# Kernel tuning notes

Measured on AMD Instinct MI355X. Metric: run time of the kernel, lower is better.

## Reference

```python
import jax, jax.numpy as jnp
import numpy as np

T, B, I, H = 512, 64, 1024, 1024


def setup_inputs() -> dict:
    key = jax.random.key(0)
    ks = jax.random.split(key, 9)
    u = lambda k, shape: jax.random.uniform(k, shape, jnp.float32, -0.05, 0.05)
    return {
        "x": jax.random.normal(ks[0], (T, B, I), jnp.float32),
        "h0": jnp.zeros((B, H), jnp.float32),
        "c0": jnp.zeros((B, H), jnp.float32),
        "W_f": u(ks[1], (I + H, H)), "b_f": u(ks[2], (H,)),
        "W_i": u(ks[3], (I + H, H)), "b_i": u(ks[4], (H,)),
        "W_C": u(ks[5], (I + H, H)), "b_C": u(ks[6], (H,)),
        "W_o": u(ks[7], (I + H, H)), "b_o": u(ks[8], (H,)),
    }


def reference(x, h0, c0, W_f, b_f, W_i, b_i, W_C, b_C, W_o, b_o):
    # Fuse the 4 gate projections into one GEMM: W is [(H_prev + I), 4H]
    W = jnp.concatenate([W_f, W_i, W_C, W_o], axis=1)  # [I+H, 4H]
    b = jnp.concatenate([b_f, b_i, b_C, b_o], axis=0)  # [4H]
    Hn = h0.shape[1]

    def step(carry, x_t):
        h_t1, c_t1 = carry
        xh = jnp.concatenate([h_t1, x_t], axis=1)  # [B, H+I]
        gates = xh @ W + b                          # [B, 4H]
        f_t = jax.nn.sigmoid(gates[:, 0 * Hn:1 * Hn])
        i_t = jax.nn.sigmoid(gates[:, 1 * Hn:2 * Hn])
        g_t = jnp.tanh(gates[:, 2 * Hn:3 * Hn])
        o_t = jax.nn.sigmoid(gates[:, 3 * Hn:4 * Hn])
        c_t = f_t * c_t1 + i_t * g_t
        h_t = o_t * jnp.tanh(c_t)
        return (h_t, c_t), h_t

    (h_last, c_last), h_seq = jax.lax.scan(step, (h0, c0), x)
    return h_seq, h_last, c_last
```

## Files before the change

kernel.cpp:

```cpp
#include <hip/hip_runtime.h>

typedef unsigned short u16;
typedef unsigned int   u32;
typedef unsigned long long u64;
typedef __attribute__((ext_vector_type(8))) __bf16 bf16x8;
typedef __attribute__((ext_vector_type(4))) float  f32x4;

#define NWG    128
#define TSTEPS 512

__device__ __forceinline__ u16 f2bf(float f) {
  union { float f; u32 u; } v; v.f = f;
  return (u16)((v.u + 0x7FFFu + ((v.u >> 16) & 1u)) >> 16);
}
__device__ __forceinline__ float sigf(float x)     { return 1.f / (1.f + __expf(-x)); }
__device__ __forceinline__ float tanhfast(float x) { return 2.f / (1.f + __expf(-2.f * x)) - 1.f; }

__global__ void convert_x_kernel(const float* __restrict__ x, u16* __restrict__ xb, long n) {
  long i = (long)(blockIdx.x * blockDim.x + threadIdx.x) * 4;
  long stride = (long)gridDim.x * blockDim.x * 4;
  for (; i < n; i += stride) {
    float4 v = *reinterpret_cast<const float4*>(x + i);
    ushort4 o; o.x = f2bf(v.x); o.y = f2bf(v.y); o.z = f2bf(v.z); o.w = f2bf(v.w);
    *reinterpret_cast<ushort4*>(xb + i) = o;
  }
}

__global__ void convert_h0_tiled(const float* __restrict__ h0, u16* __restrict__ hb) {
  int gid = blockIdx.x * blockDim.x + threadIdx.x;
  int row = gid >> 9;
  int k0  = (gid & 511) << 1;
  float a = h0[row * 1024 + k0];
  float b = h0[row * 1024 + k0 + 1];
  int off = ((row >> 4) * 32 + (k0 >> 5)) * 512 + (row & 15) * 32 + ((k0 >> 3) & 3) * 8 + (k0 & 7);
  u32 hv = (u32)f2bf(a) | ((u32)f2bf(b) << 16);
  *((u32*)hb + (off >> 1)) = hv;
}

__global__ void arrange_w_kernel(const float* __restrict__ Wf, const float* __restrict__ Wi,
                                 const float* __restrict__ Wc, const float* __restrict__ Wo,
                                 u16* __restrict__ wfrag) {
  __shared__ float lds[4][512][8];
  const int n = blockIdx.x >> 2;
  const int w = blockIdx.x & 3;
  const int tid = threadIdx.x;
  #pragma unroll
  for (int g = 0; g < 4; ++g) {
    const float* W = (g == 0) ? Wf : (g == 1) ? Wi : (g == 2) ? Wc : Wo;
    for (int it = 0; it < 16; ++it) {
      int e = it * 256 + tid;
      int kk = e >> 3, jj = e & 7;
      lds[g][kk][jj] = W[(size_t)(w * 512 + kk) * 1024 + n * 8 + jj];
    }
  }
  __syncthreads();
  u16* outp = wfrag + ((size_t)blockIdx.x << 14);
  for (int it = 0; it < 64; ++it) {
    int e = it * 256 + tid;
    int b = e & 7, lane = (e >> 3) & 63, tile = (e >> 9) & 1, ks = e >> 10;
    int kk = ks * 32 + ((lane >> 4) << 3) + b;
    int c  = tile * 16 + (lane & 15);
    int g  = c >> 3, jj = c & 7;
    outp[e] = f2bf(lds[g][kk][jj]);
  }
}

__launch_bounds__(256, 1)
__global__ void lstm_main_kernel(
    const u16* __restrict__ xbf, const u16* __restrict__ wfrag,
    const float* __restrict__ c0,
    const float* __restrict__ bF, const float* __restrict__ bI,
    const float* __restrict__ bC, const float* __restrict__ bO,
    u16* __restrict__ hb, float* __restrict__ out, u32* flags)
{
  const int n    = blockIdx.x;
  const int tid  = threadIdx.x;

  if (n == NWG) {
    if (tid < 64) {
      for (u32 tv = 1; tv < TSTEPS; ++tv) {
        while (true) {
          u32 f0 = __hip_atomic_load(flags + tid,      __ATOMIC_RELAXED, __HIP_MEMORY_SCOPE_AGENT);
          u32 f1 = __hip_atomic_load(flags + 64 + tid, __ATOMIC_RELAXED, __HIP_MEMORY_SCOPE_AGENT);
          if (__all((f0 >= tv) && (f1 >= tv))) break;
          __builtin_amdgcn_s_sleep(1);
        }
        if (tid < 8)
          __hip_atomic_store(flags + 192 + tid * 16, tv, __ATOMIC_RELAXED, __HIP_MEMORY_SCOPE_AGENT);
      }
    }
    return;
  }

  const int w    = tid >> 6;
  const int lane = tid & 63;
  const int lr   = lane & 15;
  const int hi   = lane >> 4;
  const int lk   = hi << 3;
  u32* const epoch = flags + 192 + (n & 7) * 16;

  __shared__ float part[4][64][36];
  __shared__ u32 go;

  bf16x8 bq[16][2];
  {
    const u16* wp = wfrag + ((size_t)(n * 4 + w) << 14) + lane * 8;
    #pragma unroll
    for (int ks = 0; ks < 16; ++ks) {
      bq[ks][0] = *reinterpret_cast<const bf16x8*>(wp + ks * 1024);
      bq[ks][1] = *reinterpret_cast<const bf16x8*>(wp + ks * 1024 + 512);
    }
  }
  if (tid == 0) go = 0;
  __syncthreads();

  const int erow = tid >> 2;
  const int ejj  = (tid & 3) << 1;
  const int j0   = n * 8 + ejj;
  float cR0 = c0[erow * 1024 + j0];
  float cR1 = c0[erow * 1024 + j0 + 1];
  const float bf0 = bF[j0], bf1 = bF[j0 + 1];
  const float bi0 = bI[j0], bi1 = bI[j0 + 1];
  const float bc0 = bC[j0], bc1 = bC[j0 + 1];
  const float bo0 = bO[j0], bo1 = bO[j0 + 1];
  const int hoff_u32 = (((erow >> 4) * 32 + (j0 >> 5)) * 512
                        + (erow & 15) * 32 + ((j0 >> 3) & 3) * 8 + (j0 & 7)) >> 1;

  #pragma unroll 1
  for (int t = 0; t < TSTEPS; ++t) {
    f32x4 acc[4][2];
    #pragma unroll
    for (int m = 0; m < 4; ++m) {
      acc[m][0] = (f32x4){0.f, 0.f, 0.f, 0.f};
      acc[m][1] = (f32x4){0.f, 0.f, 0.f, 0.f};
    }

    if (w < 2) {
      if (t > 0) {
        const u32 tv = (u32)t;
        if (w == 0) {
          while (__hip_atomic_load(epoch, __ATOMIC_RELAXED, __HIP_MEMORY_SCOPE_AGENT) < tv)
            __builtin_amdgcn_s_sleep(4);
          if (lane == 0)
            __hip_atomic_store(&go, tv, __ATOMIC_RELAXED, __HIP_MEMORY_SCOPE_WORKGROUP);
        } else {
          while (__hip_atomic_load(&go, __ATOMIC_RELAXED, __HIP_MEMORY_SCOPE_WORKGROUP) < tv)
            __builtin_amdgcn_s_sleep(1);
        }
      }
      const u64* hq = (const u64*)(hb + (t & 1) * 65536);
      union U { u64 q[2]; bf16x8 v; };
      U av[4][16];
      #pragma unroll
      for (int m = 0; m < 4; ++m)
        #pragma unroll
        for (int ks = 0; ks < 16; ++ks) {
          int idx = (m * 32 + w * 16 + ks) * 128 + lr * 8 + hi * 2;
          av[m][ks].q[0] = __hip_atomic_load(hq + idx,     __ATOMIC_RELAXED, __HIP_MEMORY_SCOPE_AGENT);
          av[m][ks].q[1] = __hip_atomic_load(hq + idx + 1, __ATOMIC_RELAXED, __HIP_MEMORY_SCOPE_AGENT);
        }
      __builtin_amdgcn_sched_barrier(0);
      #pragma unroll
      for (int m = 0; m < 4; ++m)
        #pragma unroll
        for (int ks = 0; ks < 16; ++ks) {
          acc[m][0] = __builtin_amdgcn_mfma_f32_16x16x32_bf16(av[m][ks].v, bq[ks][0], acc[m][0], 0, 0, 0);
          acc[m][1] = __builtin_amdgcn_mfma_f32_16x16x32_bf16(av[m][ks].v, bq[ks][1], acc[m][1], 0, 0, 0);
        }
    } else {
      const u16* asrc = xbf + (size_t)t * 65536 + (w - 2) * 512;
      #pragma unroll
      for (int ks = 0; ks < 16; ++ks) {
        #pragma unroll
        for (int m = 0; m < 4; ++m) {
          bf16x8 av = *reinterpret_cast<const bf16x8*>(asrc + (m * 16 + lr) * 1024 + ks * 32 + lk);
          acc[m][0] = __builtin_amdgcn_mfma_f32_16x16x32_bf16(av, bq[ks][0], acc[m][0], 0, 0, 0);
          acc[m][1] = __builtin_amdgcn_mfma_f32_16x16x32_bf16(av, bq[ks][1], acc[m][1], 0, 0, 0);
        }
      }
    }

    #pragma unroll
    for (int m = 0; m < 4; ++m)
      #pragma unroll
      for (int nt = 0; nt < 2; ++nt)
        #pragma unroll
        for (int r = 0; r < 4; ++r)
          part[w][m * 16 + (hi << 2) + r][nt * 16 + lr] = acc[m][nt][r];

    __syncthreads();

    float a8[8];
    #pragma unroll
    for (int q = 0; q < 2; ++q) {
      int jj = ejj + q;
      #pragma unroll
      for (int g = 0; g < 4; ++g)
        a8[q * 4 + g] = part[0][erow][g * 8 + jj] + part[1][erow][g * 8 + jj]
                      + part[2][erow][g * 8 + jj] + part[3][erow][g * 8 + jj];
    }
    float fA = sigf(a8[0] + bf0), iA = sigf(a8[1] + bi0);
    float gA = tanhfast(a8[2] + bc0), oA = sigf(a8[3] + bo0);
    float cn0 = fA * cR0 + iA * gA;
    float hn0 = oA * tanhfast(cn0);
    cR0 = cn0;
    float fB = sigf(a8[4] + bf1), iB = sigf(a8[5] + bi1);
    float gB = tanhfast(a8[6] + bc1), oB = sigf(a8[7] + bo1);
    float cn1 = fB * cR1 + iB * gB;
    float hn1 = oB * tanhfast(cn1);
    cR1 = cn1;

    {
      u32 hv = (u32)f2bf(hn0) | ((u32)f2bf(hn1) << 16);
      u32* hdst32 = (u32*)(hb + ((t + 1) & 1) * 65536) + hoff_u32;
      __hip_atomic_store(hdst32, hv, __ATOMIC_RELAXED, __HIP_MEMORY_SCOPE_AGENT);
    }

    __syncthreads();
    if (t < TSTEPS - 1 && tid == 0)
      __hip_atomic_store(flags + n, (u32)(t + 1), __ATOMIC_RELAXED, __HIP_MEMORY_SCOPE_AGENT);

    size_t ob = (size_t)t * 65536 + erow * 1024 + j0;
    out[ob]     = hn0;
    out[ob + 1] = hn1;
    if (t == TSTEPS - 1) {
      out[33554432 + erow * 1024 + j0]     = hn0;
      out[33554432 + erow * 1024 + j0 + 1] = hn1;
      out[33619968 + erow * 1024 + j0]     = cn0;
      out[33619968 + erow * 1024 + j0 + 1] = cn1;
    }
  }
}

extern "C" void kernel_launch(void* const* d_in, const int* in_sizes, int n_in,
                              void* d_out, int out_size, void* d_ws, size_t ws_size,
                              hipStream_t stream) {
  const float* x  = (const float*)d_in[0];
  const float* h0 = (const float*)d_in[1];
  const float* c0 = (const float*)d_in[2];
  const float* Wf = (const float*)d_in[3];
  const float* bf = (const float*)d_in[4];
  const float* Wi = (const float*)d_in[5];
  const float* bi = (const float*)d_in[6];
  const float* Wc = (const float*)d_in[7];
  const float* bc = (const float*)d_in[8];
  const float* Wo = (const float*)d_in[9];
  const float* bo = (const float*)d_in[10];

  if (ws_size < ((80u << 20) + (1u << 18) + 2048)) return;
  char* ws   = (char*)d_ws;
  u16* wfrag = (u16*)ws;
  u16* xbf   = (u16*)(ws + (16u << 20));
  u16* hb    = (u16*)(ws + (80u << 20));
  u32* flags = (u32*)(ws + (80u << 20) + (1u << 18));
  float* outp = (float*)d_out;

  hipMemsetAsync(flags, 0, 2048, stream);
  convert_x_kernel<<<2048, 256, 0, stream>>>(x, xbf, (long)512 * 64 * 1024);
  convert_h0_tiled<<<128, 256, 0, stream>>>(h0, hb);
  arrange_w_kernel<<<512, 256, 0, stream>>>(Wf, Wi, Wc, Wo, wfrag);

  void* args[] = {(void*)&xbf, (void*)&wfrag, (void*)&c0, (void*)&bf, (void*)&bi,
                  (void*)&bc, (void*)&bo, (void*)&hb, (void*)&outp, (void*)&flags};
  hipError_t e = hipLaunchCooperativeKernel((const void*)lstm_main_kernel, dim3(NWG + 1),
                                            dim3(256), args, 0, stream);
  if (e != hipSuccess) {
    lstm_main_kernel<<<dim3(NWG + 1), dim3(256), 0, stream>>>(xbf, wfrag, c0, bf, bi,
                                                              bc, bo, hb, outp, flags);
  }
}
```

Before: 5.674 ms.

## Halve persistent workgroups, give each 16 hidden units with doubled weight registers

```diff
diff --git a/kernel.cpp b/kernel.cpp
--- a/kernel.cpp
+++ b/kernel.cpp
@@ -6,7 +6,7 @@
 typedef __attribute__((ext_vector_type(8))) __bf16 bf16x8;
 typedef __attribute__((ext_vector_type(4))) float  f32x4;
 
-#define NWG    128
+#define NWG    64
 #define TSTEPS 512
 
 __device__ __forceinline__ u16 f2bf(float f) {
@@ -40,28 +40,26 @@
 __global__ void arrange_w_kernel(const float* __restrict__ Wf, const float* __restrict__ Wi,
                                  const float* __restrict__ Wc, const float* __restrict__ Wo,
                                  u16* __restrict__ wfrag) {
-  __shared__ float lds[4][512][8];
+  __shared__ float lds[512][16];
   const int n = blockIdx.x >> 2;
   const int w = blockIdx.x & 3;
   const int tid = threadIdx.x;
-  #pragma unroll
+  u16* outp = wfrag + ((size_t)blockIdx.x << 15);
   for (int g = 0; g < 4; ++g) {
     const float* W = (g == 0) ? Wf : (g == 1) ? Wi : (g == 2) ? Wc : Wo;
-    for (int it = 0; it < 16; ++it) {
+    __syncthreads();
+    for (int it = 0; it < 32; ++it) {
       int e = it * 256 + tid;
-      int kk = e >> 3, jj = e & 7;
-      lds[g][kk][jj] = W[(size_t)(w * 512 + kk) * 1024 + n * 8 + jj];
-    }
-  }
-  __syncthreads();
-  u16* outp = wfrag + ((size_t)blockIdx.x << 14);
-  for (int it = 0; it < 64; ++it) {
-    int e = it * 256 + tid;
-    int b = e & 7, lane = (e >> 3) & 63, tile = (e >> 9) & 1, ks = e >> 10;
-    int kk = ks * 32 + ((lane >> 4) << 3) + b;
-    int c  = tile * 16 + (lane & 15);
-    int g  = c >> 3, jj = c & 7;
-    outp[e] = f2bf(lds[g][kk][jj]);
+      int kk = e >> 4, jj = e & 15;
+      lds[kk][jj] = W[(size_t)(w * 512 + kk) * 1024 + n * 16 + jj];
+    }
+    __syncthreads();
+    for (int it = 0; it < 32; ++it) {
+      int e = it * 256 + tid;
+      int b = e & 7, lane = (e >> 3) & 63, ks = e >> 9;
+      int kk = ks * 32 + ((lane >> 4) << 3) + b;
+      outp[(ks * 4 + g) * 512 + lane * 8 + b] = f2bf(lds[kk][lane & 15]);
+    }
   }
 }
 
@@ -80,9 +78,8 @@
     if (tid < 64) {
       for (u32 tv = 1; tv < TSTEPS; ++tv) {
         while (true) {
-          u32 f0 = __hip_atomic_load(flags + tid,      __ATOMIC_RELAXED, __HIP_MEMORY_SCOPE_AGENT);
-          u32 f1 = __hip_atomic_load(flags + 64 + tid, __ATOMIC_RELAXED, __HIP_MEMORY_SCOPE_AGENT);
-          if (__all((f0 >= tv) && (f1 >= tv))) break;
+          u32 f0 = __hip_atomic_load(flags + tid, __ATOMIC_RELAXED, __HIP_MEMORY_SCOPE_AGENT);
+          if (__all(f0 >= tv)) break;
           __builtin_amdgcn_s_sleep(1);
         }
         if (tid < 8)
@@ -99,41 +96,42 @@
   const int lk   = hi << 3;
   u32* const epoch = flags + 192 + (n & 7) * 16;
 
-  __shared__ float part[4][64][36];
+  __shared__ float part[4][64][72];
   __shared__ u32 go;
 
-  bf16x8 bq[16][2];
+  bf16x8 bq[16][4];
   {
-    const u16* wp = wfrag + ((size_t)(n * 4 + w) << 14) + lane * 8;
-    #pragma unroll
-    for (int ks = 0; ks < 16; ++ks) {
-      bq[ks][0] = *reinterpret_cast<const bf16x8*>(wp + ks * 1024);
-      bq[ks][1] = *reinterpret_cast<const bf16x8*>(wp + ks * 1024 + 512);
-    }
+    const u16* wp = wfrag + ((size_t)(n * 4 + w) << 15) + lane * 8;
+    #pragma unroll
+    for (int ks = 0; ks < 16; ++ks)
+      #pragma unroll
+      for (int g = 0; g < 4; ++g)
+        bq[ks][g] = *reinterpret_cast<const bf16x8*>(wp + (ks * 4 + g) * 512);
   }
   if (tid == 0) go = 0;
   __syncthreads();
 
   const int erow = tid >> 2;
-  const int ejj  = (tid & 3) << 1;
-  const int j0   = n * 8 + ejj;
-  float cR0 = c0[erow * 1024 + j0];
-  float cR1 = c0[erow * 1024 + j0 + 1];
-  const float bf0 = bF[j0], bf1 = bF[j0 + 1];
-  const float bi0 = bI[j0], bi1 = bI[j0 + 1];
-  const float bc0 = bC[j0], bc1 = bC[j0 + 1];
-  const float bo0 = bO[j0], bo1 = bO[j0 + 1];
-  const int hoff_u32 = (((erow >> 4) * 32 + (j0 >> 5)) * 512
-                        + (erow & 15) * 32 + ((j0 >> 3) & 3) * 8 + (j0 & 7)) >> 1;
+  const int jq   = (tid & 3) << 2;
+  const int j0   = n * 16 + jq;
+  float cR[4], bFv[4], bIv[4], bCv[4], bOv[4];
+  #pragma unroll
+  for (int jj = 0; jj < 4; ++jj) {
+    cR[jj]  = c0[erow * 1024 + j0 + jj];
+    bFv[jj] = bF[j0 + jj]; bIv[jj] = bI[j0 + jj];
+    bCv[jj] = bC[j0 + jj]; bOv[jj] = bO[j0 + jj];
+  }
+  const int hoff16 = ((erow >> 4) * 32 + (j0 >> 5)) * 512
+                     + (erow & 15) * 32 + (j0 & 31);
 
   #pragma unroll 1
   for (int t = 0; t < TSTEPS; ++t) {
-    f32x4 acc[4][2];
-    #pragma unroll
-    for (int m = 0; m < 4; ++m) {
-      acc[m][0] = (f32x4){0.f, 0.f, 0.f, 0.f};
-      acc[m][1] = (f32x4){0.f, 0.f, 0.f, 0.f};
-    }
+    f32x4 acc[4][4];
+    #pragma unroll
+    for (int m = 0; m < 4; ++m)
+      #pragma unroll
+      for (int g = 0; g < 4; ++g)
+        acc[m][g] = (f32x4){0.f, 0.f, 0.f, 0.f};
 
     if (w < 2) {
       if (t > 0) {
@@ -149,24 +147,21 @@
         }
       }
       const u64* hq = (const u64*)(hb + (t & 1) * 65536);
-      union U { u64 q[2]; bf16x8 v; };
-      U av[4][16];
-      #pragma unroll
-      for (int m = 0; m < 4; ++m)
+      #pragma unroll
+      for (int m = 0; m < 4; ++m) {
+        union { u64 q[2]; bf16x8 v; } av[16];
         #pragma unroll
         for (int ks = 0; ks < 16; ++ks) {
           int idx = (m * 32 + w * 16 + ks) * 128 + lr * 8 + hi * 2;
-          av[m][ks].q[0] = __hip_atomic_load(hq + idx,     __ATOMIC_RELAXED, __HIP_MEMORY_SCOPE_AGENT);
-          av[m][ks].q[1] = __hip_atomic_load(hq + idx + 1, __ATOMIC_RELAXED, __HIP_MEMORY_SCOPE_AGENT);
-        }
-      __builtin_amdgcn_sched_barrier(0);
-      #pragma unroll
-      for (int m = 0; m < 4; ++m)
-        #pragma unroll
-        for (int ks = 0; ks < 16; ++ks) {
-          acc[m][0] = __builtin_amdgcn_mfma_f32_16x16x32_bf16(av[m][ks].v, bq[ks][0], acc[m][0], 0, 0, 0);
-          acc[m][1] = __builtin_amdgcn_mfma_f32_16x16x32_bf16(av[m][ks].v, bq[ks][1], acc[m][1], 0, 0, 0);
-        }
+          av[ks].q[0] = __hip_atomic_load(hq + idx,     __ATOMIC_RELAXED, __HIP_MEMORY_SCOPE_AGENT);
+          av[ks].q[1] = __hip_atomic_load(hq + idx + 1, __ATOMIC_RELAXED, __HIP_MEMORY_SCOPE_AGENT);
+        }
+        #pragma unroll
+        for (int ks = 0; ks < 16; ++ks)
+          #pragma unroll
+          for (int g = 0; g < 4; ++g)
+            acc[m][g] = __builtin_amdgcn_mfma_f32_16x16x32_bf16(av[ks].v, bq[ks][g], acc[m][g], 0, 0, 0);
+      }
     } else {
       const u16* asrc = xbf + (size_t)t * 65536 + (w - 2) * 512;
       #pragma unroll
@@ -174,8 +169,9 @@
         #pragma unroll
         for (int m = 0; m < 4; ++m) {
           bf16x8 av = *reinterpret_cast<const bf16x8*>(asrc + (m * 16 + lr) * 1024 + ks * 32 + lk);
-          acc[m][0] = __builtin_amdgcn_mfma_f32_16x16x32_bf16(av, bq[ks][0], acc[m][0], 0, 0, 0);
-          acc[m][1] = __builtin_amdgcn_mfma_f32_16x16x32_bf16(av, bq[ks][1], acc[m][1], 0, 0, 0);
+          #pragma unroll
+          for (int g = 0; g < 4; ++g)
+            acc[m][g] = __builtin_amdgcn_mfma_f32_16x16x32_bf16(av, bq[ks][g], acc[m][g], 0, 0, 0);
         }
       }
     }
@@ -183,37 +179,34 @@
     #pragma unroll
     for (int m = 0; m < 4; ++m)
       #pragma unroll
-      for (int nt = 0; nt < 2; ++nt)
+      for (int g = 0; g < 4; ++g)
         #pragma unroll
         for (int r = 0; r < 4; ++r)
-          part[w][m * 16 + (hi << 2) + r][nt * 16 + lr] = acc[m][nt][r];
-
-    __syncthreads();
-
-    float a8[8];
-    #pragma unroll
-    for (int q = 0; q < 2; ++q) {
-      int jj = ejj + q;
-      #pragma unroll
-      for (int g = 0; g < 4; ++g)
-        a8[q * 4 + g] = part[0][erow][g * 8 + jj] + part[1][erow][g * 8 + jj]
-                      + part[2][erow][g * 8 + jj] + part[3][erow][g * 8 + jj];
-    }
-    float fA = sigf(a8[0] + bf0), iA = sigf(a8[1] + bi0);
-    float gA = tanhfast(a8[2] + bc0), oA = sigf(a8[3] + bo0);
-    float cn0 = fA * cR0 + iA * gA;
-    float hn0 = oA * tanhfast(cn0);
-    cR0 = cn0;
-    float fB = sigf(a8[4] + bf1), iB = sigf(a8[5] + bi1);
-    float gB = tanhfast(a8[6] + bc1), oB = sigf(a8[7] + bo1);
-    float cn1 = fB * cR1 + iB * gB;
-    float hn1 = oB * tanhfast(cn1);
-    cR1 = cn1;
+          part[w][m * 16 + (hi << 2) + r][g * 16 + lr] = acc[m][g][r];
+
+    __syncthreads();
+
+    float hn[4], cnv[4];
+    #pragma unroll
+    for (int jj = 0; jj < 4; ++jj) {
+      float a4[4];
+      #pragma unroll
+      for (int g = 0; g < 4; ++g)
+        a4[g] = part[0][erow][g * 16 + jq + jj] + part[1][erow][g * 16 + jq + jj]
+              + part[2][erow][g * 16 + jq + jj] + part[3][erow][g * 16 + jq + jj];
+      float fA = sigf(a4[0] + bFv[jj]), iA = sigf(a4[1] + bIv[jj]);
+      float gA = tanhfast(a4[2] + bCv[jj]), oA = sigf(a4[3] + bOv[jj]);
+      float cn = fA * cR[jj] + iA * gA;
+      hn[jj] = oA * tanhfast(cn);
+      cnv[jj] = cn;
+      cR[jj] = cn;
+    }
 
     {
-      u32 hv = (u32)f2bf(hn0) | ((u32)f2bf(hn1) << 16);
-      u32* hdst32 = (u32*)(hb + ((t + 1) & 1) * 65536) + hoff_u32;
-      __hip_atomic_store(hdst32, hv, __ATOMIC_RELAXED, __HIP_MEMORY_SCOPE_AGENT);
+      u64 hv = (u64)f2bf(hn[0]) | ((u64)f2bf(hn[1]) << 16)
+             | ((u64)f2bf(hn[2]) << 32) | ((u64)f2bf(hn[3]) << 48);
+      u64* hdst = (u64*)(hb + ((t + 1) & 1) * 65536) + (hoff16 >> 2);
+      __hip_atomic_store(hdst, hv, __ATOMIC_RELAXED, __HIP_MEMORY_SCOPE_AGENT);
     }
 
     __syncthreads();
@@ -221,13 +214,12 @@
       __hip_atomic_store(flags + n, (u32)(t + 1), __ATOMIC_RELAXED, __HIP_MEMORY_SCOPE_AGENT);
 
     size_t ob = (size_t)t * 65536 + erow * 1024 + j0;
-    out[ob]     = hn0;
-    out[ob + 1] = hn1;
+    *reinterpret_cast<float4*>(out + ob) = (float4){hn[0], hn[1], hn[2], hn[3]};
     if (t == TSTEPS - 1) {
-      out[33554432 + erow * 1024 + j0]     = hn0;
-      out[33554432 + erow * 1024 + j0 + 1] = hn1;
-      out[33619968 + erow * 1024 + j0]     = cn0;
-      out[33619968 + erow * 1024 + j0 + 1] = cn1;
+      *reinterpret_cast<float4*>(out + 33554432 + erow * 1024 + j0) =
+          (float4){hn[0], hn[1], hn[2], hn[3]};
+      *reinterpret_cast<float4*>(out + 33619968 + erow * 1024 + j0) =
+          (float4){cnv[0], cnv[1], cnv[2], cnv[3]};
     }
   }
 }
@@ -258,7 +250,7 @@
   hipMemsetAsync(flags, 0, 2048, stream);
   convert_x_kernel<<<2048, 256, 0, stream>>>(x, xbf, (long)512 * 64 * 1024);
   convert_h0_tiled<<<128, 256, 0, stream>>>(h0, hb);
-  arrange_w_kernel<<<512, 256, 0, stream>>>(Wf, Wi, Wc, Wo, wfrag);
+  arrange_w_kernel<<<256, 256, 0, stream>>>(Wf, Wi, Wc, Wo, wfrag);
 
   void* args[] = {(void*)&xbf, (void*)&wfrag, (void*)&c0, (void*)&bf, (void*)&bi,
                   (void*)&bc, (void*)&bo, (void*)&hb, (void*)&outp, (void*)&flags};
```

Measured after the change: 9.582 ms. 68.9% more time.
